# Kernel tuning notes

Hardware: AMD Instinct MI355X
Metric: run time of the kernel (lower is better)

## Reference

```python
import jax, jax.numpy as jnp
import numpy as np

B, S, H = 1, 2048, 4096
N_HEADS, N_KV, HEAD_DIM = 32, 8, 128
ROPE_THETA = 10000.0


def setup_inputs() -> dict:
    key = jax.random.key(0)
    k1, k2, k3 = jax.random.split(key, 3)
    hidden_states = jax.random.normal(k1, (B, S, H), dtype=jnp.float32)
    # fused QKV projection weight: rows = (n_heads + 2*n_kv_heads) * head_dim
    Wqkv = jax.random.normal(k2, ((N_HEADS + 2 * N_KV) * HEAD_DIM, H), dtype=jnp.float32) * 0.02
    Wo = jax.random.normal(k3, (H, N_HEADS * HEAD_DIM), dtype=jnp.float32) * 0.02
    return {"hidden_states": hidden_states, "Wqkv": Wqkv, "Wo": Wo}


def _rope_tables(seqlen, dim, theta):
    inv_freq = 1.0 / (theta ** (jnp.arange(0, dim, 2, dtype=jnp.float32) / dim))  # [dim/2]
    t = jnp.arange(seqlen, dtype=jnp.float32)
    freqs = jnp.outer(t, inv_freq)  # [S, dim/2]
    return jnp.cos(freqs), jnp.sin(freqs)


def _apply_rope(x, cos, sin):
    # torch code: reshape(...,2,-1).transpose -> view_as_complex pairs (x[j], x[j+d/2])
    # i.e. NeoX rotate-half on first/second halves of head_dim.
    d2 = x.shape[-1] // 2
    x1, x2 = x[..., :d2], x[..., d2:]
    c = cos[None, :, None, :]  # [1,S,1,d/2]
    s = sin[None, :, None, :]
    return jnp.concatenate([x1 * c - x2 * s, x1 * s + x2 * c], axis=-1)


def reference(hidden_states, Wqkv, Wo):
    b, s, h = hidden_states.shape
    # fused QKV projection
    qkv = jnp.einsum('bsh,oh->bso', hidden_states, Wqkv)
    q_end = N_HEADS * HEAD_DIM
    k_end = q_end + N_KV * HEAD_DIM
    xq = qkv[..., :q_end].reshape(b, s, N_HEADS, HEAD_DIM)
    xk = qkv[..., q_end:k_end].reshape(b, s, N_KV, HEAD_DIM)
    xv = qkv[..., k_end:].reshape(b, s, N_KV, HEAD_DIM)
    # RoPE (start_pos = 0 prefill)
    cos, sin = _rope_tables(s, HEAD_DIM, ROPE_THETA)
    xq = _apply_rope(xq, cos, sin)
    xk = _apply_rope(xk, cos, sin)
    # GQA: expand kv heads to query heads (head h uses kv head h // groups)
    groups = N_HEADS // N_KV
    xk = jnp.repeat(xk, groups, axis=2)  # [b,s,nH,hd]
    xv = jnp.repeat(xv, groups, axis=2)
    # causal attention, softmax scale 1/sqrt(head_dim) (flash_attn default, softcap=0)
    scale = 1.0 / jnp.sqrt(jnp.float32(HEAD_DIM))
    scores = jnp.einsum('bqhd,bkhd->bhqk', xq, xk) * scale
    causal = jnp.tril(jnp.ones((s, s), dtype=bool))
    scores = jnp.where(causal[None, None, :, :], scores, jnp.float32(-1e30))
    probs = jax.nn.softmax(scores, axis=-1)
    out = jnp.einsum('bhqk,bkhd->bqhd', probs, xv).reshape(b, s, N_HEADS * HEAD_DIM)
    attn_output = jnp.einsum('bsd,hd->bsh', out, Wo)
    return attn_output
```

## Files before the change

### kernel.cpp

```cpp
#include <hip/hip_runtime.h>
#include <stdint.h>

typedef unsigned short u16;
typedef unsigned int   u32;
typedef short bf16x8 __attribute__((ext_vector_type(8)));
typedef float f32x4  __attribute__((ext_vector_type(4)));

template <int N> struct IC { static constexpr int value = N; };

__device__ __forceinline__ u16 f2bf(float f) {
    union { float f; u32 u; } v; v.f = f;
    u32 u = v.u;
    u32 r = (u + 0x7fffu + ((u >> 16) & 1u)) >> 16;
    return (u16)r;
}
__device__ __forceinline__ float bf2f(u16 h) {
    union { u32 u; float f; } v; v.u = ((u32)h) << 16;
    return v.f;
}

__device__ __forceinline__ void gload_lds16(const void* g, void* l) {
    __builtin_amdgcn_global_load_lds(
        (__attribute__((address_space(1))) void*)g,
        (__attribute__((address_space(3))) void*)l,
        16, 0, 0);
}

__global__ __launch_bounds__(256) void cvt_all(const float4* __restrict__ s1, uint2* __restrict__ d1,
                                               const float4* __restrict__ s2, uint2* __restrict__ d2,
                                               const float4* __restrict__ s3, uint2* __restrict__ d3) {
    const float4* s; uint2* d; int i;
    int b = blockIdx.x;
    if (b < 8192)        { s = s1; d = d1; i = b * 256 + threadIdx.x; }
    else if (b < 32768)  { s = s2; d = d2; i = (b - 8192) * 256 + threadIdx.x; }
    else                 { s = s3; d = d3; i = (b - 32768) * 256 + threadIdx.x; }
    float4 v = s[i];
    uint2 o;
    o.x = (u32)f2bf(v.x) | ((u32)f2bf(v.y) << 16);
    o.y = (u32)f2bf(v.z) | ((u32)f2bf(v.w) << 16);
    d[i] = o;
}

template <typename OUT_T>
__global__ __launch_bounds__(512, 2) void gemm_bt8(const u16* __restrict__ A,
                                                   const u16* __restrict__ B,
                                                   OUT_T* __restrict__ C,
                                                   int M, int N, int K) {
    __shared__ u16 As[2][256 * 64];
    __shared__ u16 Bs[2][256 * 64];

    const int tid  = threadIdx.x;
    const int lane = tid & 63;
    const int wv   = tid >> 6;
    const int row0 = blockIdx.y * 256;
    const int col0 = blockIdx.x * 256;

    const int fr = lane & 15;
    const int fq = lane >> 4;
    const int u0 = (fq ^ (fr & 7)) * 8;
    const int u1 = u0 ^ 32;

    const int sr  = tid >> 3;
    const int scp = tid & 7;
    const int sgc = scp ^ (sr & 7);

    const int wrr = (wv >> 2) * 64;
    const int wcc = (wv & 3) * 32;

    f32x4 acc[2][2][4][2];
#pragma unroll
    for (int a = 0; a < 2; ++a)
#pragma unroll
        for (int b = 0; b < 2; ++b)
#pragma unroll
            for (int c = 0; c < 4; ++c)
#pragma unroll
                for (int d = 0; d < 2; ++d) acc[a][b][c][d] = f32x4{0.f, 0.f, 0.f, 0.f};

    auto stageA = [&](int buf, int half, int kt) {
#pragma unroll
        for (int j = 0; j < 2; ++j) {
            int r = j * 64 + sr;
            gload_lds16(A + (size_t)(row0 + half * 128 + r) * K + kt * 64 + sgc * 8,
                        &As[buf][(half * 128 + r) * 64 + scp * 8]);
        }
    };
    auto stageB = [&](int buf, int half, int kt) {
#pragma unroll
        for (int j = 0; j < 2; ++j) {
            int r = j * 64 + sr;
            gload_lds16(B + (size_t)(col0 + half * 128 + r) * K + kt * 64 + sgc * 8,
                        &Bs[buf][(half * 128 + r) * 64 + scp * 8]);
        }
    };

    auto phase = [&](auto BUFc, auto MQc, auto NQc, int vmEnd, auto&& stg) {
        constexpr int BUF = decltype(BUFc)::value;
        constexpr int MQ  = decltype(MQc)::value;
        constexpr int NQ  = decltype(NQc)::value;
        const u16* as_ = &As[BUF][(MQ * 128 + wrr + fr) * 64];
        const u16* bs_ = &Bs[BUF][(NQ * 128 + wcc + fr) * 64];
        bf16x8 af[4][2], bfv[2][2];
#pragma unroll
        for (int im = 0; im < 4; ++im) {
            af[im][0] = *(const bf16x8*)&as_[im * 1024 + u0];
            af[im][1] = *(const bf16x8*)&as_[im * 1024 + u1];
        }
#pragma unroll
        for (int in = 0; in < 2; ++in) {
            bfv[in][0] = *(const bf16x8*)&bs_[in * 1024 + u0];
            bfv[in][1] = *(const bf16x8*)&bs_[in * 1024 + u1];
        }
        stg();
        __builtin_amdgcn_s_barrier();
        asm volatile("s_waitcnt lgkmcnt(0)" ::: "memory");
        __builtin_amdgcn_sched_barrier(0);
        __builtin_amdgcn_s_setprio(1);
#pragma unroll
        for (int im = 0; im < 4; ++im)
#pragma unroll
            for (int in = 0; in < 2; ++in) {
                acc[MQ][NQ][im][in] = __builtin_amdgcn_mfma_f32_16x16x32_bf16(
                    af[im][0], bfv[in][0], acc[MQ][NQ][im][in], 0, 0, 0);
                acc[MQ][NQ][im][in] = __builtin_amdgcn_mfma_f32_16x16x32_bf16(
                    af[im][1], bfv[in][1], acc[MQ][NQ][im][in], 0, 0, 0);
            }
        __builtin_amdgcn_s_setprio(0);
        if (vmEnd == 4)      asm volatile("s_waitcnt vmcnt(4)" ::: "memory");
        else if (vmEnd == 0) asm volatile("s_waitcnt vmcnt(0)" ::: "memory");
        __builtin_amdgcn_s_barrier();
    };

    const int nkt = K >> 6;
    const int nit = nkt >> 1;

    stageA(0, 0, 0); stageB(0, 0, 0); stageA(0, 1, 0); stageB(0, 1, 0);
    stageA(1, 0, 1); stageB(1, 0, 1);
    asm volatile("s_waitcnt vmcnt(4)" ::: "memory");
    __builtin_amdgcn_s_barrier();

    for (int it = 0; it < nit; ++it) {
        const int t1 = 2 * it + 1;
        const int t2 = 2 * it + 2;
        const int t3 = t2 + 1;
        const bool h2 = t2 < nkt, h3 = t3 < nkt;
        phase(IC<0>{}, IC<0>{}, IC<0>{}, -1,          [&] { stageA(1, 1, t1); });
        phase(IC<0>{}, IC<0>{}, IC<1>{}, -1,          [&] { stageB(1, 1, t1); });
        phase(IC<0>{}, IC<1>{}, IC<0>{}, -1,          [&] { if (h2) stageA(0, 0, t2); });
        phase(IC<0>{}, IC<1>{}, IC<1>{}, h2 ? 4 : 0,  [&] { if (h2) stageB(0, 0, t2); });
        phase(IC<1>{}, IC<0>{}, IC<0>{}, -1,          [&] { if (h2) stageA(0, 1, t2); });
        phase(IC<1>{}, IC<0>{}, IC<1>{}, -1,          [&] { if (h2) stageB(0, 1, t2); });
        phase(IC<1>{}, IC<1>{}, IC<0>{}, -1,          [&] { if (h3) stageA(1, 0, t3); });
        phase(IC<1>{}, IC<1>{}, IC<1>{}, 4,           [&] { if (h3) stageB(1, 0, t3); });
    }

    const int orow = (lane >> 4) * 4;
    const int ocol = lane & 15;
#pragma unroll
    for (int mq = 0; mq < 2; ++mq)
#pragma unroll
        for (int nq = 0; nq < 2; ++nq)
#pragma unroll
            for (int im = 0; im < 4; ++im)
#pragma unroll
                for (int in = 0; in < 2; ++in)
#pragma unroll
                    for (int r = 0; r < 4; ++r) {
                        int mm = row0 + mq * 128 + wrr + im * 16 + orow + r;
                        int nn = col0 + nq * 128 + wcc + in * 16 + ocol;
                        float v = acc[mq][nq][im][in][r];
                        if constexpr (sizeof(OUT_T) == 2)
                            C[(size_t)mm * N + nn] = (OUT_T)f2bf(v);
                        else
                            C[(size_t)mm * N + nn] = (OUT_T)v;
                    }
}

__global__ __launch_bounds__(256) void prep_kv(const u16* __restrict__ qkv,
                                               u16* __restrict__ Kb,
                                               u16* __restrict__ Vt) {
    if (blockIdx.x < 4096) {
        int id = blockIdx.x * 256 + threadIdx.x;
        int d  = id & 63;
        int t  = id >> 6;
        int kh = t & 7;
        int s  = t >> 3;
        const size_t rowbase = (size_t)s * 6144 + 4096;
        float inv = __expf(-(float)d * (9.210340371976184f / 64.0f));
        float ang = (float)s * inv;
        float cs, sn; __sincosf(ang, &sn, &cs);
        float x1 = bf2f(qkv[rowbase + kh * 128 + d]);
        float x2 = bf2f(qkv[rowbase + kh * 128 + d + 64]);
        size_t o = ((size_t)kh * 2048 + s) * 128 + d;
        Kb[o]      = f2bf(x1 * cs - x2 * sn);
        Kb[o + 64] = f2bf(x1 * sn + x2 * cs);
    } else {
        int id = (blockIdx.x - 4096) * 256 + threadIdx.x;
        int s8 = id & 255;
        int d  = (id >> 8) & 127;
        int vh = id >> 15;
        u16 tmp[8];
#pragma unroll
        for (int j = 0; j < 8; ++j)
            tmp[j] = qkv[(size_t)(s8 * 8 + j) * 6144 + 5120 + vh * 128 + d];
        *(uint4*)(Vt + ((size_t)vh * 128 + d) * 2048 + s8 * 8) = *(uint4*)tmp;
    }
}

__device__ __forceinline__ void softmax_pack(f32x4 s[4], bool diag, int w, int m, int quad,
                                             float sl2e, float& lsum, bf16x8 af[2]) {
#pragma unroll
    for (int nt = 0; nt < 4; ++nt)
#pragma unroll
        for (int r = 0; r < 4; ++r) {
            float p = __builtin_amdgcn_exp2f(s[nt][r] * sl2e);
            if (diag && (nt * 16 + quad * 4 + r > w * 16 + m)) p = 0.f;
            s[nt][r] = p;
            lsum += p;
        }
#pragma unroll
    for (int kk2 = 0; kk2 < 2; ++kk2)
#pragma unroll
        for (int ws = 0; ws < 2; ++ws) {
            u32 a, b;
            asm("v_cvt_pk_bf16_f32 %0, %1, %2"
                : "=v"(a) : "v"(s[2 * kk2][2 * ws]), "v"(s[2 * kk2][2 * ws + 1]));
            asm("v_cvt_pk_bf16_f32 %0, %1, %2"
                : "=v"(b) : "v"(s[2 * kk2 + 1][2 * ws]), "v"(s[2 * kk2 + 1][2 * ws + 1]));
            asm("v_permlane32_swap_b32 %0, %1" : "+v"(a), "+v"(b));
            asm("v_permlane16_swap_b32 %0, %1" : "+v"(a), "+v"(b));
            ((u32*)&af[kk2])[ws]     = a;
            ((u32*)&af[kk2])[ws + 2] = b;
        }
}

template <bool TWO>
__device__ __forceinline__ void attn_pass2(const bf16x8 qfA[4], const bf16x8 qfB[4],
                                           f32x4 accA[8], f32x4 accB[8],
                                           float& lA, float& lB,
                                           const u16* Ks, const u16* Vs,
                                           int w, int m, int quad,
                                           bool diagA, bool diagB, float sl2e) {
    f32x4 sA[4], sB[4];
#pragma unroll
    for (int nt = 0; nt < 4; ++nt) {
        sA[nt] = f32x4{0.f, 0.f, 0.f, 0.f};
        sB[nt] = f32x4{0.f, 0.f, 0.f, 0.f};
    }

    __builtin_amdgcn_s_setprio(1);
#pragma unroll
    for (int kk = 0; kk < 4; ++kk)
#pragma unroll
        for (int nt = 0; nt < 4; ++nt) {
            int pos = (kk * 4 + quad) ^ (m & 7);
            bf16x8 b = *(const bf16x8*)&Ks[(nt * 16 + m) * 128 + pos * 8];
            sB[nt] = __builtin_amdgcn_mfma_f32_16x16x32_bf16(b, qfB[kk], sB[nt], 0, 0, 0);
            if constexpr (TWO)
                sA[nt] = __builtin_amdgcn_mfma_f32_16x16x32_bf16(b, qfA[kk], sA[nt], 0, 0, 0);
        }
    __builtin_amdgcn_s_setprio(0);

    bf16x8 afA[2], afB[2];
    softmax_pack(sB, diagB, w, m, quad, sl2e, lB, afB);
    if constexpr (TWO) softmax_pack(sA, diagA, w, m, quad, sl2e, lA, afA);

    __builtin_amdgcn_s_setprio(1);
#pragma unroll
    for (int kk2 = 0; kk2 < 2; ++kk2)
#pragma unroll
        for (int nt = 0; nt < 8; ++nt) {
            int pos = (kk2 * 4 + quad) ^ (m & 7);
            bf16x8 b = *(const bf16x8*)&Vs[(nt * 16 + m) * 64 + pos * 8];
            accB[nt] = __builtin_amdgcn_mfma_f32_16x16x32_bf16(afB[kk2], b, accB[nt], 0, 0, 0);
            if constexpr (TWO)
                accA[nt] = __builtin_amdgcn_mfma_f32_16x16x32_bf16(afA[kk2], b, accA[nt], 0, 0, 0);
        }
    __builtin_amdgcn_s_setprio(0);
}

__global__ __launch_bounds__(256, 2) void attn_mfma(const u16* __restrict__ qkv,
                                                    const u16* __restrict__ Kb,
                                                    const u16* __restrict__ Vt,
                                                    u16* __restrict__ ctx) {
    __shared__ u16 Ks[2][64 * 128];
    __shared__ u16 Vs[2][128 * 64];

    const int tid  = threadIdx.x;
    const int lane = tid & 63;
    const int w    = tid >> 6;
    const int m    = lane & 15;
    const int quad = lane >> 4;
    const int h    = blockIdx.y;
    const int kh   = h >> 2;
    const int qtA  = blockIdx.x;
    const int qtB  = 31 - qtA;

    const u16* Ktile0 = Kb + (size_t)kh * 2048 * 128;
    const u16* Vtile0 = Vt + (size_t)kh * 128 * 2048;
    const float sl2e = 0.08838834764831845f * 1.4426950408889634f;

    auto stage = [&](int buf, int kt) {
        const u16* Kt = Ktile0 + (size_t)kt * 64 * 128;
#pragma unroll
        for (int i = 0; i < 4; ++i) {
            int slot = i * 256 + tid;
            int row = slot >> 4, cp = slot & 15;
            int gc = cp ^ (row & 7);
            gload_lds16(Kt + row * 128 + gc * 8, &Ks[buf][slot * 8]);
        }
        const u16* Vtt = Vtile0 + kt * 64;
#pragma unroll
        for (int i = 0; i < 4; ++i) {
            int slot = i * 256 + tid;
            int row = slot >> 3, cp = slot & 7;
            int gc = cp ^ (row & 7);
            gload_lds16(Vtt + (size_t)row * 2048 + gc * 8, &Vs[buf][slot * 8]);
        }
    };

    bf16x8 qa[4], qb[4];
#pragma unroll
    for (int which = 0; which < 2; ++which) {
        const int qt = which ? qtB : qtA;
        const int s  = qt * 64 + w * 16 + m;
        bf16x8 raw[4];
        const u16* qp = qkv + (size_t)s * 6144 + h * 128 + quad * 8;
#pragma unroll
        for (int kk = 0; kk < 4; ++kk)
            raw[kk] = *(const bf16x8*)(qp + kk * 32);
        bf16x8* dst = which ? qb : qa;
#pragma unroll
        for (int half = 0; half < 2; ++half)
#pragma unroll
            for (int j = 0; j < 8; ++j) {
                int d = half * 32 + quad * 8 + j;
                float inv = __expf(-(float)d * (9.210340371976184f / 64.0f));
                float ang = (float)s * inv;
                float cs, sn; __sincosf(ang, &sn, &cs);
                float x1 = bf2f(((const u16*)&raw[half])[j]);
                float x2 = bf2f(((const u16*)&raw[half + 2])[j]);
                ((u16*)&dst[half])[j]     = f2bf(x1 * cs - x2 * sn);
                ((u16*)&dst[half + 2])[j] = f2bf(x1 * sn + x2 * cs);
            }
    }

    f32x4 accA[8], accB[8];
#pragma unroll
    for (int i = 0; i < 8; ++i) { accA[i] = f32x4{0.f, 0.f, 0.f, 0.f}; accB[i] = f32x4{0.f, 0.f, 0.f, 0.f}; }
    float lA = 0.f, lB = 0.f;

    stage(0, 0);
    for (int kt = 0; kt <= qtB; ++kt) {
        __syncthreads();
        if (kt < qtB) stage((kt + 1) & 1, kt + 1);

        const u16* ks = Ks[kt & 1];
        const u16* vs = Vs[kt & 1];
        if (kt <= qtA)
            attn_pass2<true >(qa, qb, accA, accB, lA, lB, ks, vs, w, m, quad,
                              kt == qtA, false, sl2e);
        else
            attn_pass2<false>(qa, qb, accA, accB, lA, lB, ks, vs, w, m, quad,
                              false, kt == qtB, sl2e);
    }

#pragma unroll
    for (int which = 0; which < 2; ++which) {
        const int qt  = which ? qtB : qtA;
        f32x4*   acc  = which ? accB : accA;
        float    l    = which ? lB   : lA;
        l += __shfl_xor(l, 16);
        l += __shfl_xor(l, 32);
        float linv[4];
#pragma unroll
        for (int r = 0; r < 4; ++r)
            linv[r] = 1.f / __shfl(l, quad * 4 + r);
#pragma unroll
        for (int r = 0; r < 4; ++r) {
            size_t rowg = (size_t)(qt * 64 + w * 16 + quad * 4 + r);
#pragma unroll
            for (int nt = 0; nt < 8; ++nt)
                ctx[rowg * 4096 + h * 128 + nt * 16 + m] = f2bf(acc[nt][r] * linv[r]);
        }
    }
}

extern "C" void kernel_launch(void* const* d_in, const int* in_sizes, int n_in,
                              void* d_out, int out_size, void* d_ws, size_t ws_size,
                              hipStream_t stream) {
    const float* hs   = (const float*)d_in[0];
    const float* wqkv = (const float*)d_in[1];
    const float* wo   = (const float*)d_in[2];
    float* out = (float*)d_out;

    char* ws = (char*)d_ws;
    u16* hA  = (u16*)ws;  ws += (size_t)2048 * 4096 * 2;
    u16* wQ  = (u16*)ws;  ws += (size_t)6144 * 4096 * 2;
    u16* wO  = (u16*)ws;  ws += (size_t)4096 * 4096 * 2;
    u16* qkv = (u16*)ws;  ws += (size_t)2048 * 6144 * 2;
    u16* Kb  = (u16*)ws;  ws += (size_t)8 * 2048 * 128 * 2;
    u16* Vt  = (u16*)ws;  ws += (size_t)8 * 128 * 2048 * 2;
    u16* ctx = (u16*)ws;  ws += (size_t)2048 * 4096 * 2;

    cvt_all<<<49152, 256, 0, stream>>>((const float4*)hs,   (uint2*)hA,
                                       (const float4*)wqkv, (uint2*)wQ,
                                       (const float4*)wo,   (uint2*)wO);

    gemm_bt8<u16><<<dim3(24, 8), 512, 0, stream>>>(hA, wQ, qkv, 2048, 6144, 4096);

    prep_kv<<<5120, 256, 0, stream>>>(qkv, Kb, Vt);

    attn_mfma<<<dim3(16, 32), 256, 0, stream>>>(qkv, Kb, Vt, ctx);

    gemm_bt8<float><<<dim3(16, 8), 512, 0, stream>>>(ctx, wO, out, 2048, 4096, 4096);
}
```

Measured before the change: 598.1 us.

## Reuse LDS fragments across GEMM phases and remap workgroups for XCD locality

The GEMM kernel now keeps the A and B register fragments loaded from LDS across consecutive phases instead of re-reading both for every 128x128 sub-tile. This cuts LDS read traffic per K-step from eight A and eight B fragment loads to two A and four B, at the cost of more live VGPRs. The launch also moves to a 1D grid with a swizzle that sends consecutive blocks to the same XCD, so neighbouring tiles that share rows or columns of the operands hit the same L2 slice.

```diff
diff --git a/kernel.cpp b/kernel.cpp
--- a/kernel.cpp
+++ b/kernel.cpp
@@ -52,8 +52,12 @@
     const int tid  = threadIdx.x;
     const int lane = tid & 63;
     const int wv   = tid >> 6;
-    const int row0 = blockIdx.y * 256;
-    const int col0 = blockIdx.x * 256;
+
+    const int nwg = gridDim.x;
+    const int nx  = N >> 8;
+    const int swz = ((int)blockIdx.x & 7) * (nwg >> 3) + ((int)blockIdx.x >> 3);
+    const int row0 = (swz / nx) * 256;
+    const int col0 = (swz % nx) * 256;
 
     const int fr = lane & 15;
     const int fq = lane >> 4;
@@ -77,6 +81,42 @@
 #pragma unroll
                 for (int d = 0; d < 2; ++d) acc[a][b][c][d] = f32x4{0.f, 0.f, 0.f, 0.f};
 
+    bf16x8 af[4][2];
+    bf16x8 bfv[2][2][2];
+
+    auto readA = [&](int buf, int mq) {
+        const u16* as_ = &As[buf][(mq * 128 + wrr + fr) * 64];
+#pragma unroll
+        for (int im = 0; im < 4; ++im) {
+            af[im][0] = *(const bf16x8*)&as_[im * 1024 + u0];
+            af[im][1] = *(const bf16x8*)&as_[im * 1024 + u1];
+        }
+    };
+    auto readB = [&](int buf, auto NQc) {
+        constexpr int NQ = decltype(NQc)::value;
+        const u16* bs_ = &Bs[buf][(NQ * 128 + wcc + fr) * 64];
+#pragma unroll
+        for (int in = 0; in < 2; ++in) {
+            bfv[NQ][in][0] = *(const bf16x8*)&bs_[in * 1024 + u0];
+            bfv[NQ][in][1] = *(const bf16x8*)&bs_[in * 1024 + u1];
+        }
+    };
+    auto mfma16 = [&](auto MQc, auto NQc) {
+        constexpr int MQ = decltype(MQc)::value;
+        constexpr int NQ = decltype(NQc)::value;
+        __builtin_amdgcn_s_setprio(1);
+#pragma unroll
+        for (int im = 0; im < 4; ++im)
+#pragma unroll
+            for (int in = 0; in < 2; ++in) {
+                acc[MQ][NQ][im][in] = __builtin_amdgcn_mfma_f32_16x16x32_bf16(
+                    af[im][0], bfv[NQ][in][0], acc[MQ][NQ][im][in], 0, 0, 0);
+                acc[MQ][NQ][im][in] = __builtin_amdgcn_mfma_f32_16x16x32_bf16(
+                    af[im][1], bfv[NQ][in][1], acc[MQ][NQ][im][in], 0, 0, 0);
+            }
+        __builtin_amdgcn_s_setprio(0);
+    };
+
     auto stageA = [&](int buf, int half, int kt) {
 #pragma unroll
         for (int j = 0; j < 2; ++j) {
@@ -94,38 +134,13 @@
         }
     };
 
-    auto phase = [&](auto BUFc, auto MQc, auto NQc, int vmEnd, auto&& stg) {
-        constexpr int BUF = decltype(BUFc)::value;
-        constexpr int MQ  = decltype(MQc)::value;
-        constexpr int NQ  = decltype(NQc)::value;
-        const u16* as_ = &As[BUF][(MQ * 128 + wrr + fr) * 64];
-        const u16* bs_ = &Bs[BUF][(NQ * 128 + wcc + fr) * 64];
-        bf16x8 af[4][2], bfv[2][2];
-#pragma unroll
-        for (int im = 0; im < 4; ++im) {
-            af[im][0] = *(const bf16x8*)&as_[im * 1024 + u0];
-            af[im][1] = *(const bf16x8*)&as_[im * 1024 + u1];
-        }
-#pragma unroll
-        for (int in = 0; in < 2; ++in) {
-            bfv[in][0] = *(const bf16x8*)&bs_[in * 1024 + u0];
-            bfv[in][1] = *(const bf16x8*)&bs_[in * 1024 + u1];
-        }
+    auto phase = [&](auto&& rds, auto&& stg, auto MQc, auto NQc, int vmEnd) {
+        rds();
         stg();
         __builtin_amdgcn_s_barrier();
         asm volatile("s_waitcnt lgkmcnt(0)" ::: "memory");
         __builtin_amdgcn_sched_barrier(0);
-        __builtin_amdgcn_s_setprio(1);
-#pragma unroll
-        for (int im = 0; im < 4; ++im)
-#pragma unroll
-            for (int in = 0; in < 2; ++in) {
-                acc[MQ][NQ][im][in] = __builtin_amdgcn_mfma_f32_16x16x32_bf16(
-                    af[im][0], bfv[in][0], acc[MQ][NQ][im][in], 0, 0, 0);
-                acc[MQ][NQ][im][in] = __builtin_amdgcn_mfma_f32_16x16x32_bf16(
-                    af[im][1], bfv[in][1], acc[MQ][NQ][im][in], 0, 0, 0);
-            }
-        __builtin_amdgcn_s_setprio(0);
+        mfma16(MQc, NQc);
         if (vmEnd == 4)      asm volatile("s_waitcnt vmcnt(4)" ::: "memory");
         else if (vmEnd == 0) asm volatile("s_waitcnt vmcnt(0)" ::: "memory");
         __builtin_amdgcn_s_barrier();
@@ -144,14 +159,22 @@
         const int t2 = 2 * it + 2;
         const int t3 = t2 + 1;
         const bool h2 = t2 < nkt, h3 = t3 < nkt;
-        phase(IC<0>{}, IC<0>{}, IC<0>{}, -1,          [&] { stageA(1, 1, t1); });
-        phase(IC<0>{}, IC<0>{}, IC<1>{}, -1,          [&] { stageB(1, 1, t1); });
-        phase(IC<0>{}, IC<1>{}, IC<0>{}, -1,          [&] { if (h2) stageA(0, 0, t2); });
-        phase(IC<0>{}, IC<1>{}, IC<1>{}, h2 ? 4 : 0,  [&] { if (h2) stageB(0, 0, t2); });
-        phase(IC<1>{}, IC<0>{}, IC<0>{}, -1,          [&] { if (h2) stageA(0, 1, t2); });
-        phase(IC<1>{}, IC<0>{}, IC<1>{}, -1,          [&] { if (h2) stageB(0, 1, t2); });
-        phase(IC<1>{}, IC<1>{}, IC<0>{}, -1,          [&] { if (h3) stageA(1, 0, t3); });
-        phase(IC<1>{}, IC<1>{}, IC<1>{}, 4,           [&] { if (h3) stageB(1, 0, t3); });
+        phase([&] { readA(0, 0); readB(0, IC<0>{}); }, [&] { stageA(1, 1, t1); },
+              IC<0>{}, IC<0>{}, -1);
+        phase([&] { readB(0, IC<1>{}); },              [&] { stageB(1, 1, t1); },
+              IC<0>{}, IC<1>{}, -1);
+        phase([&] { readA(0, 1); },                    [&] { if (h2) stageA(0, 0, t2); },
+              IC<1>{}, IC<0>{}, -1);
+        phase([&] {},                                  [&] { if (h2) stageB(0, 0, t2); },
+              IC<1>{}, IC<1>{}, h2 ? 4 : 0);
+        phase([&] { readA(1, 0); readB(1, IC<0>{}); }, [&] { if (h2) stageA(0, 1, t2); },
+              IC<0>{}, IC<0>{}, -1);
+        phase([&] { readB(1, IC<1>{}); },              [&] { if (h2) stageB(0, 1, t2); },
+              IC<0>{}, IC<1>{}, -1);
+        phase([&] { readA(1, 1); },                    [&] { if (h3) stageA(1, 0, t3); },
+              IC<1>{}, IC<0>{}, -1);
+        phase([&] {},                                  [&] { if (h3) stageB(1, 0, t3); },
+              IC<1>{}, IC<1>{}, 4);
     }
 
     const int orow = (lane >> 4) * 4;
@@ -407,11 +430,11 @@
                                        (const float4*)wqkv, (uint2*)wQ,
                                        (const float4*)wo,   (uint2*)wO);
 
-    gemm_bt8<u16><<<dim3(24, 8), 512, 0, stream>>>(hA, wQ, qkv, 2048, 6144, 4096);
+    gemm_bt8<u16><<<192, 512, 0, stream>>>(hA, wQ, qkv, 2048, 6144, 4096);
 
     prep_kv<<<5120, 256, 0, stream>>>(qkv, Kb, Vt);
 
     attn_mfma<<<dim3(16, 32), 256, 0, stream>>>(qkv, Kb, Vt, ctx);
 
-    gemm_bt8<float><<<dim3(16, 8), 512, 0, stream>>>(ctx, wO, out, 2048, 4096, 4096);
-}
+    gemm_bt8<float><<<128, 512, 0, stream>>>(ctx, wO, out, 2048, 4096, 4096);
+}
```

Measured after the change: 542.0 us. 1.1x faster.
